# Optimization experiments

Hardware: AMD Instinct MI355X
Metric: run time of the kernel (lower is better)

The kernel has to match this reference:

```python
import jax, jax.numpy as jnp
import numpy as np

B, T, N = 512, 200, 256
ENC_G, ENC_C = 256, 256
C_DIM, G_DIM, U_DIM, F_DIM = 128, 256, 64, 64
CLIP = 5.0


def _gru(x, h, Wih, Whh, bih, bhh):
    # PyTorch nn.GRUCell math
    gi = x @ Wih.T + bih
    gh = h @ Whh.T + bhh
    ir, iz, inn = jnp.split(gi, 3, axis=-1)
    hr, hz, hn = jnp.split(gh, 3, axis=-1)
    r = jax.nn.sigmoid(ir + hr)
    z = jax.nn.sigmoid(iz + hz)
    n = jnp.tanh(inn + r * hn)
    return (1.0 - z) * n + z * h


def setup_inputs() -> dict:
    key = jax.random.key(0)
    ks = iter(jax.random.split(key, 64))

    def gru_p(i, h):
        return (jax.random.normal(next(ks), (3 * h, i)) * i ** -0.5,
                jax.random.normal(next(ks), (3 * h, h)) * h ** -0.5,
                jnp.zeros(3 * h), jnp.zeros(3 * h))

    def lin_p(i, o):
        return (jax.random.normal(next(ks), (o, i)) * i ** -0.5, jnp.zeros(o))

    inp = {}
    inp['x'] = jax.random.uniform(next(ks), (B, T, N))
    inp['eps_g0'] = jax.random.normal(next(ks), (B, G_DIM))
    inp['eps_u'] = jax.random.normal(next(ks), (B, T, U_DIM))
    for name, (i, h) in [('gf', (N, ENC_G)), ('gb', (N, ENC_G)),
                         ('cf', (N, ENC_C)), ('cb', (N, ENC_C)),
                         ('ct', (2 * ENC_C + F_DIM, C_DIM)), ('gn', (U_DIM, G_DIM))]:
        Wih, Whh, bih, bhh = gru_p(i, h)
        inp['Wih_' + name] = Wih; inp['Whh_' + name] = Whh
        inp['bih_' + name] = bih; inp['bhh_' + name] = bhh
    for name, (i, o) in [('g0m', (2 * ENC_G, G_DIM)), ('g0v', (2 * ENC_G, G_DIM)),
                         ('um', (C_DIM, U_DIM)), ('uv', (C_DIM, U_DIM)),
                         ('f', (G_DIM, F_DIM)), ('r', (F_DIM, N))]:
        W, b = lin_p(i, o)
        inp['W_' + name] = W; inp['b_' + name] = b
    return inp


def reference(x, eps_g0, eps_u,
              Wih_gf, Whh_gf, bih_gf, bhh_gf,
              Wih_gb, Whh_gb, bih_gb, bhh_gb,
              Wih_cf, Whh_cf, bih_cf, bhh_cf,
              Wih_cb, Whh_cb, bih_cb, bhh_cb,
              Wih_ct, Whh_ct, bih_ct, bhh_ct,
              Wih_gn, Whh_gn, bih_gn, bhh_gn,
              W_g0m, b_g0m, W_g0v, b_g0v,
              W_um, b_um, W_uv, b_uv,
              W_f, b_f, W_r, b_r):
    Bsz = x.shape[0]
    xs = x.transpose(1, 0, 2)  # [T, B, N]
    zg = jnp.zeros((Bsz, ENC_G), x.dtype)
    zc = jnp.zeros((Bsz, ENC_C), x.dtype)

    def make_enc(pg, pc):
        def step(carry, xt):
            hg, hc = carry
            hg = jnp.minimum(_gru(xt, hg, *pg), CLIP)   # clamp(max=clip_val)
            hc = jnp.minimum(_gru(xt, hc, *pc), CLIP)
            return (hg, hc), hc
        return step

    (hgf, _), hcf = jax.lax.scan(
        make_enc((Wih_gf, Whh_gf, bih_gf, bhh_gf), (Wih_cf, Whh_cf, bih_cf, bhh_cf)),
        (zg, zc), xs)
    (hgb, _), hcb = jax.lax.scan(
        make_enc((Wih_gb, Whh_gb, bih_gb, bhh_gb), (Wih_cb, Whh_cb, bih_cb, bhh_cb)),
        (zg, zc), xs[::-1])
    h_enc_g = jnp.concatenate([hgf, hgb], axis=-1)        # [B, 2*ENC_G]
    h_enc_c = jnp.concatenate([hcf, hcb[::-1]], axis=-1)  # [T, B, 2*ENC_C]

    g0_mean = h_enc_g @ W_g0m.T + b_g0m
    g0_logv = jnp.log(jnp.exp(h_enc_g @ W_g0v.T + b_g0v) + 1e-4)
    g0 = eps_g0 * jnp.exp(0.5 * g0_logv) + g0_mean

    f0 = g0 @ W_f.T + b_f
    hc0 = jnp.zeros((Bsz, C_DIM), x.dtype)

    def gen_step(carry, inp):
        h_c, g, f = carry
        henc_t, eps_t = inp
        cin = jnp.concatenate([henc_t, f], axis=-1)
        h_c = jnp.clip(_gru(cin, h_c, Wih_ct, Whh_ct, bih_ct, bhh_ct), 0.0, CLIP)
        um = h_c @ W_um.T + b_um
        ul = h_c @ W_uv.T + b_uv
        u = eps_t * jnp.exp(0.5 * ul) + um
        g = jnp.clip(_gru(u, g, Wih_gn, Whh_gn, bih_gn, bhh_gn), 0.0, CLIP)
        f = g @ W_f.T + b_f
        return (h_c, g, f), (um, ul, f)

    _, (u_means, u_logvs, factors) = jax.lax.scan(
        gen_step, (hc0, g0, f0), (h_enc_c, eps_u.transpose(1, 0, 2)))
    factors = factors.transpose(1, 0, 2)  # [B, T, F_DIM]
    rates = jnp.exp(jnp.clip(factors @ W_r.T + b_r, -CLIP, CLIP))
    return (g0_mean, g0_logv,
            u_means.transpose(1, 0, 2), u_logvs.transpose(1, 0, 2),
            factors, rates)
```

## Files before the change

### kernel.cpp

```cpp
#include <hip/hip_runtime.h>
#include <hip/hip_bf16.h>
#include <stdint.h>

typedef __bf16 bf16x8 __attribute__((ext_vector_type(8)));
typedef __bf16 bf16x4 __attribute__((ext_vector_type(4)));
typedef float  f32x4  __attribute__((ext_vector_type(4)));
typedef unsigned short u16x8 __attribute__((ext_vector_type(8)));

#define MFMA_B16(A_,B_,C_) __builtin_amdgcn_mfma_f32_16x16x32_bf16((A_),(B_),(C_),0,0,0)

static constexpr int TT = 200;
static constexpr int TC = 25;
static constexpr int NCH = 8;

static __device__ __forceinline__ float sig_f(float x){ return 1.f/(1.f+__expf(-x)); }
static __device__ __forceinline__ float tanh_f(float x){
  float e = __expf(-2.f*fabsf(x));
  float t = (1.f-e)/(1.f+e);
  return x<0.f ? -t : t;
}
static __device__ __forceinline__ float bf2f(unsigned short u){
  union{unsigned int i; float f;} v; v.i = ((unsigned)u)<<16; return v.f;
}
static __device__ __forceinline__ void pin8(bf16x8 &v){ asm volatile("" : "+v"(v)); }

static __device__ __forceinline__ int swz_off(int row, int col_bytes, int strideB){
  return (row*strideB + col_bytes) ^ ((row&7)<<4);
}
static __device__ __forceinline__ bf16x8 lds_rdA(const __bf16* buf, int row, int kt, int lq, int strideB){
  return *(const bf16x8*)((const char*)buf + swz_off(row, kt*64 + lq*16, strideB));
}
static __device__ __forceinline__ void lds_wr(__bf16* buf, int row, int dim, int strideB, float v){
  *(__bf16*)((char*)buf + swz_off(row, dim*2, strideB)) = (__bf16)v;
}
static __device__ __forceinline__ void lds_barrier(){
  asm volatile("s_waitcnt lgkmcnt(0)" ::: "memory");
  __builtin_amdgcn_s_barrier();
}

__global__ void cvt_bf16(const float* __restrict__ s, __bf16* __restrict__ d, int n){
  int i = blockIdx.x*blockDim.x + threadIdx.x;
  int st = gridDim.x*blockDim.x;
  for(; i<n; i+=st) d[i] = (__bf16)s[i];
}

__global__ void epsT_k(const float4* __restrict__ e, float4* __restrict__ o){
  const int total = 512*200*16;
  int j = blockIdx.x*blockDim.x + threadIdx.x;
  int st = gridDim.x*blockDim.x;
  for(; j<total; j+=st){
    int b = j/3200, rem = j - b*3200;
    int t = rem>>4, dq = rem&15;
    o[((size_t)t*512 + b)*16 + dq] = e[j];
  }
}

__global__ __launch_bounds__(256) void gi_gemm(const float* __restrict__ x,
                                               const __bf16* __restrict__ Wall,
                                               __bf16* __restrict__ gi, int t0){
  const int tid=threadIdx.x, w=tid>>6, l=tid&63, lr=l&15, lq=l>>4;
  const int cell = blockIdx.y;
  const bool fwd = (cell&1)==0;
  const int m0 = blockIdx.x*64;
  const int tloc = m0>>9, b0 = m0&511;
  const int tabs = fwd ? (t0+tloc) : (TT-1-(t0+tloc));
  const int brow = b0 + w*16 + lr;

  const float* xp = x + (size_t)brow*TT*256 + (size_t)tabs*256 + lq*8;
  bf16x8 a[8];
  #pragma unroll
  for(int kt=0;kt<8;kt++){
    float4 f0 = *(const float4*)(xp + kt*32);
    float4 f1 = *(const float4*)(xp + kt*32 + 4);
    bf16x8 v;
    v[0]=(__bf16)f0.x; v[1]=(__bf16)f0.y; v[2]=(__bf16)f0.z; v[3]=(__bf16)f0.w;
    v[4]=(__bf16)f1.x; v[5]=(__bf16)f1.y; v[6]=(__bf16)f1.z; v[7]=(__bf16)f1.w;
    a[kt]=v;
  }
  const __bf16* Wc = Wall + (size_t)cell*768*256;
  #pragma unroll 1
  for(int nt=0;nt<48;nt++){
    f32x4 acc={};
    const __bf16* bp = Wc + (size_t)(nt*16+lr)*256 + lq*8;
    #pragma unroll
    for(int kt=0;kt<8;kt++)
      acc = MFMA_B16(a[kt], *(const bf16x8*)(bp + kt*32), acc);
    bf16x4 pk;
    pk[0]=(__bf16)acc[0]; pk[1]=(__bf16)acc[1]; pk[2]=(__bf16)acc[2]; pk[3]=(__bf16)acc[3];
    *(bf16x4*)(gi + (((size_t)cell*TC + tloc)*768 + nt*16+lr)*512 + b0 + w*16 + lq*4) = pk;
  }
}

struct EncP{
  const __bf16* whh;
  const float*  bih[4];
  const float*  bhh[4];
  const __bf16* gi;
  __bf16* henc;
  float*  hcar;
  int t0;
};
__attribute__((amdgpu_waves_per_eu(2,2)))
__global__ __launch_bounds__(512) void enc_scan(EncP P){
  const int tid=threadIdx.x, w=tid>>6, l=tid&63, lr=l&15, lq=l>>4;
  const int cell=blockIdx.y, b0=blockIdx.x*16;
  const bool fwd = (cell&1)==0;
  const bool isC = cell>=2;
  const int dim0 = w*32;

  __shared__ __align__(16) __bf16 hA[2][16*256];
  __shared__ __align__(16) __bf16 giL[2][768*16];
  __shared__ float blds[1024];

  for(int d=tid; d<256; d+=512){
    blds[d]     = P.bih[cell][d]     + P.bhh[cell][d];
    blds[256+d] = P.bih[cell][256+d] + P.bhh[cell][256+d];
    blds[512+d] = P.bih[cell][512+d];
    blds[768+d] = P.bhh[cell][512+d];
  }
  const __bf16* Wh = P.whh + (size_t)cell*768*256;
  bf16x8 wreg[2][2][8];
  #pragma unroll
  for(int jt=0;jt<2;jt++)
    #pragma unroll
    for(int g=0;g<2;g++)
      #pragma unroll
      for(int kt=0;kt<8;kt++){
        wreg[jt][g][kt] = *(const bf16x8*)(Wh + (size_t)(g*256 + dim0 + jt*16 + lr)*256 + kt*32 + lq*8);
        pin8(wreg[jt][g][kt]);
      }
  f32x4 hold[2];
  #pragma unroll
  for(int jt=0;jt<2;jt++)
    #pragma unroll
    for(int rr=0;rr<4;rr++){
      float v = P.hcar[((size_t)cell*512 + b0 + lq*4+rr)*256 + dim0 + jt*16 + lr];
      hold[jt][rr] = v;
      lds_wr(hA[0], lq*4+rr, dim0+jt*16+lr, 512, v);
    }
  const int prow = w*96 + (l>>1), phal = l&1;
  const __bf16* gbase = P.gi + ((size_t)cell*TC*768 + prow)*512 + b0 + phal*8;
  u16x8 pf0, pf1, pf2;
  pf0 = *(const u16x8*)(gbase + (size_t)0*768*512 +  0*512);
  pf1 = *(const u16x8*)(gbase + (size_t)0*768*512 + 32*512);
  pf2 = *(const u16x8*)(gbase + (size_t)0*768*512 + 64*512);
  __syncthreads();
  {
    __bf16* gl = giL[0] + prow*16 + phal*8;
    *(u16x8*)(gl)        = pf0;
    *(u16x8*)(gl+32*16)  = pf1;
    *(u16x8*)(gl+64*16)  = pf2;
  }
  { int sn = 1 < TC ? 1 : TC-1;
    pf0 = *(const u16x8*)(gbase + (size_t)sn*768*512 +  0*512);
    pf1 = *(const u16x8*)(gbase + (size_t)sn*768*512 + 32*512);
    pf2 = *(const u16x8*)(gbase + (size_t)sn*768*512 + 64*512);
  }
  lds_barrier();

  int p=0, q=0;
  #pragma unroll 1
  for(int s=0;s<TC;s++){
    const int tglob = P.t0 + s;
    const int tx = fwd ? tglob : (TT-1-tglob);
    if(s+1<TC){
      __bf16* gl = giL[1-q] + prow*16 + phal*8;
      *(u16x8*)(gl)        = pf0;
      *(u16x8*)(gl+32*16)  = pf1;
      *(u16x8*)(gl+64*16)  = pf2;
    }
    { int sn = (s+2<TC) ? s+2 : TC-1;
      pf0 = *(const u16x8*)(gbase + (size_t)sn*768*512 +  0*512);
      pf1 = *(const u16x8*)(gbase + (size_t)sn*768*512 + 32*512);
      pf2 = *(const u16x8*)(gbase + (size_t)sn*768*512 + 64*512);
    }
    const __bf16* gq = giL[q];
    #pragma unroll
    for(int jt=0;jt<2;jt++){
      const int d = dim0 + jt*16 + lr;
      const __bf16* whN = Wh + (size_t)(512 + d)*256 + lq*8;
      f32x4 aR={}, aZ={}, aH={};
      #pragma unroll
      for(int kt=0;kt<8;kt++){
        bf16x8 frag = lds_rdA(hA[p], lr, kt, lq, 512);
        aR = MFMA_B16(frag, wreg[jt][0][kt], aR);
        aZ = MFMA_B16(frag, wreg[jt][1][kt], aZ);
        aH = MFMA_B16(frag, *(const bf16x8*)(whN + kt*32), aH);
      }
      ushort4 gR = *(const ushort4*)(gq + (0*256+d)*16 + lq*4);
      ushort4 gZ = *(const ushort4*)(gq + (1*256+d)*16 + lq*4);
      ushort4 gN = *(const ushort4*)(gq + (2*256+d)*16 + lq*4);
      const float bR=blds[d], bZ=blds[256+d], bI=blds[512+d], bH=blds[768+d];
      const unsigned short* uR=(const unsigned short*)&gR;
      const unsigned short* uZ=(const unsigned short*)&gZ;
      const unsigned short* uN=(const unsigned short*)&gN;
      #pragma unroll
      for(int rr=0;rr<4;rr++){
        float r = sig_f(aR[rr] + bf2f(uR[rr]) + bR);
        float z = sig_f(aZ[rr] + bf2f(uZ[rr]) + bZ);
        float nn= tanh_f(bf2f(uN[rr]) + bI + r*(aH[rr] + bH));
        float h = (1.f-z)*nn + z*hold[jt][rr];
        h = fminf(h, 5.f);
        hold[jt][rr] = h;
        lds_wr(hA[1-p], lq*4+rr, d, 512, h);
      }
    }
    if(isC){
      const int row = l>>2, dgrp = (l&3)*8;
      bf16x8 hv = *(const bf16x8*)((const char*)hA[1-p] +
                    ((row*512 + (dim0+dgrp)*2) ^ ((row&7)<<4)));
      *(bf16x8*)(P.henc + ((size_t)tx*512 + b0 + row)*512 + (cell==3?256:0) + dim0 + dgrp) = hv;
    }
    lds_barrier();
    p ^= 1; q ^= 1;
  }
  #pragma unroll
  for(int jt=0;jt<2;jt++)
    #pragma unroll
    for(int rr=0;rr<4;rr++)
      P.hcar[((size_t)cell*512 + b0 + lq*4+rr)*256 + dim0 + jt*16 + lr] = hold[jt][rr];
}

__global__ void g0_kernel(const float* __restrict__ hgf, const float* __restrict__ hgb,
                          const float* __restrict__ Wm, const float* __restrict__ bm,
                          const float* __restrict__ Wv, const float* __restrict__ bv,
                          const float* __restrict__ eps,
                          float* __restrict__ o_mean, float* __restrict__ o_logv,
                          float* __restrict__ g0){
  int j = blockIdx.x*blockDim.x + threadIdx.x;
  int b = j>>8, d = j&255;
  const float4* hf=(const float4*)(hgf + (size_t)b*256);
  const float4* hb=(const float4*)(hgb + (size_t)b*256);
  const float4* mp=(const float4*)(Wm + (size_t)d*512);
  const float4* vp=(const float4*)(Wv + (size_t)d*512);
  float am=0.f, av=0.f;
  #pragma unroll 4
  for(int k=0;k<64;k++){
    float4 h=hf[k], m=mp[k], v=vp[k];
    am += h.x*m.x + h.y*m.y + h.z*m.z + h.w*m.w;
    av += h.x*v.x + h.y*v.y + h.z*v.z + h.w*v.w;
  }
  #pragma unroll 4
  for(int k=0;k<64;k++){
    float4 h=hb[k], m=mp[64+k], v=vp[64+k];
    am += h.x*m.x + h.y*m.y + h.z*m.z + h.w*m.w;
    av += h.x*v.x + h.y*v.y + h.z*v.z + h.w*v.w;
  }
  float mean = am + bm[d];
  float ev   = __expf(av + bv[d]) + 1e-4f;
  float lv   = __logf(ev);
  o_mean[j]=mean; o_logv[j]=lv;
  g0[j] = eps[j]*sqrtf(ev) + mean;
}

__global__ __launch_bounds__(256,2) void gict_gemm(const __bf16* __restrict__ henc,
                                                   const __bf16* __restrict__ wct,
                                                   __bf16* __restrict__ gictT){
  const int tid=threadIdx.x, w=tid>>6, l=tid&63, lr=l&15, lq=l>>4;
  const int m0 = blockIdx.x*8 + w*2;
  bf16x8 a[2][16];
  #pragma unroll
  for(int m=0;m<2;m++){
    const __bf16* ap = henc + (size_t)((m0+m)*16 + lr)*512 + lq*8;
    #pragma unroll
    for(int kt=0;kt<16;kt++) a[m][kt] = *(const bf16x8*)(ap + kt*32);
  }
  #pragma unroll 1
  for(int nt=0;nt<24;nt++){
    f32x4 c0={}, c1={};
    const __bf16* bp = wct + (size_t)(nt*16+lr)*576 + lq*8;
    #pragma unroll
    for(int kt=0;kt<16;kt++){
      bf16x8 bb = *(const bf16x8*)(bp + kt*32);
      c0 = MFMA_B16(a[0][kt], bb, c0);
      c1 = MFMA_B16(a[1][kt], bb, c1);
    }
    #pragma unroll
    for(int m=0;m<2;m++){
      f32x4 c = m? c1 : c0;
      int R0 = (m0+m)*16 + lq*4;
      int t  = R0>>9, b = R0&511;
      bf16x4 pk;
      pk[0]=(__bf16)c[0]; pk[1]=(__bf16)c[1]; pk[2]=(__bf16)c[2]; pk[3]=(__bf16)c[3];
      *(bf16x4*)(gictT + ((size_t)t*384 + nt*16+lr)*512 + b) = pk;
    }
  }
}

struct GenP{
  const __bf16 *wct, *whh_ct, *wih_gn, *whh_gn, *w_um, *w_uv, *w_f;
  const float  *bih_ct, *bhh_ct, *bih_gn, *bhh_gn, *b_um, *b_uv, *b_f;
  const __bf16* gihT;
  const float*  g0;
  const float*  epsT;
  float *o_um, *o_ul, *o_f;
};
__attribute__((amdgpu_waves_per_eu(2,2)))
__global__ __launch_bounds__(512) void gen_scan(GenP P){
  const int tid=threadIdx.x, w=tid>>6, l=tid&63, lr=l&15, lq=l>>4;
  const int b0 = blockIdx.x*16;

  __shared__ __align__(16) __bf16 wgnL[768*64];
  __shared__ __align__(16) __bf16 hcA[2][16*128];
  __shared__ __align__(16) __bf16 gA [2][16*256];
  __shared__ __align__(16) __bf16 uA [16*64];
  __shared__ __align__(16) __bf16 fA [16*64];

  for(int c=tid; c<6144; c+=512){
    int row = c>>3, part = c&7;
    bf16x8 v = *(const bf16x8*)(P.wih_gn + (size_t)row*64 + part*8);
    *(bf16x8*)((char*)wgnL + ((row*128 + part*16) ^ ((row&7)<<4))) = v;
  }
  bf16x8 wrz[2][2][8];
  #pragma unroll
  for(int jt=0;jt<2;jt++)
    #pragma unroll
    for(int g=0;g<2;g++)
      #pragma unroll
      for(int kt=0;kt<8;kt++){
        wrz[jt][g][kt] = *(const bf16x8*)(P.whh_gn + (size_t)(g*256 + w*32 + jt*16 + lr)*256 + kt*32 + lq*8);
        pin8(wrz[jt][g][kt]);
      }

  const int dct = w*16 + lr;
  const int duu = (w&3)*16 + lr;
  const float bctR = P.bih_ct[dct]     + P.bhh_ct[dct];
  const float bctZ = P.bih_ct[128+dct] + P.bhh_ct[128+dct];
  const float bctI = P.bih_ct[256+dct];
  const float bctH = P.bhh_ct[256+dct];
  float bgnR[2], bgnZ[2], bgnI[2], bgnH[2];
  #pragma unroll
  for(int jt=0;jt<2;jt++){
    int d = w*32 + jt*16 + lr;
    bgnR[jt] = P.bih_gn[d]     + P.bhh_gn[d];
    bgnZ[jt] = P.bih_gn[256+d] + P.bhh_gn[256+d];
    bgnI[jt] = P.bih_gn[512+d];
    bgnH[jt] = P.bhh_gn[512+d];
  }
  const float bum = P.b_um[duu], buv = P.b_uv[duu], bff = P.b_f[duu];

  f32x4 gC[2], hcC;
  hcC = (f32x4){};
  #pragma unroll
  for(int jt=0;jt<2;jt++)
    #pragma unroll
    for(int rr=0;rr<4;rr++){
      float v = P.g0[(size_t)(b0+lq*4+rr)*256 + w*32 + jt*16 + lr];
      gC[jt][rr] = v;
      lds_wr(gA[0], lq*4+rr, w*32+jt*16+lr, 512, v);
    }
  for(int i=tid;i<16*128;i+=512) hcA[0][i] = (__bf16)0.f;
  __syncthreads();
  if(w>=4){
    f32x4 fa={};
    #pragma unroll
    for(int kt=0;kt<8;kt++){
      bf16x8 gf = lds_rdA(gA[0], lr, kt, lq, 512);
      fa = MFMA_B16(gf, *(const bf16x8*)(P.w_f + (size_t)duu*256 + kt*32 + lq*8), fa);
    }
    #pragma unroll
    for(int rr=0;rr<4;rr++) lds_wr(fA, lq*4+rr, duu, 128, fa[rr]+bff);
  }
  ushort4 gpR, gpZ, gpN; float epf[4];
  gpR = *(const ushort4*)(P.gihT + ((size_t)0*384 +       dct)*512 + b0 + lq*4);
  gpZ = *(const ushort4*)(P.gihT + ((size_t)0*384 + 128 + dct)*512 + b0 + lq*4);
  gpN = *(const ushort4*)(P.gihT + ((size_t)0*384 + 256 + dct)*512 + b0 + lq*4);
  if(w<4){
    #pragma unroll
    for(int rr=0;rr<4;rr++) epf[rr] = P.epsT[((size_t)0*512 + b0+lq*4+rr)*64 + duu];
  }
  bf16x8 cwh[3][4];
  #pragma unroll
  for(int g=0;g<3;g++)
    #pragma unroll
    for(int kt=0;kt<4;kt++)
      cwh[g][kt] = *(const bf16x8*)(P.whh_ct + (size_t)(g*128+dct)*128 + kt*32 + lq*8);
  __syncthreads();

  int pc=0, pg=0;
  #pragma unroll 1
  for(int t=0;t<TT;t++){
    {
      bf16x8 ff0 = lds_rdA(fA, lr, 0, lq, 128);
      bf16x8 ff1 = lds_rdA(fA, lr, 1, lq, 128);
      bf16x8 hp0 = lds_rdA(hcA[pc], lr, 0, lq, 256);
      bf16x8 hp1 = lds_rdA(hcA[pc], lr, 1, lq, 256);
      bf16x8 hp2 = lds_rdA(hcA[pc], lr, 2, lq, 256);
      bf16x8 hp3 = lds_rdA(hcA[pc], lr, 3, lq, 256);
      f32x4 aR={}, aZ={}, aI={}, aH={};
      #pragma unroll
      for(int g=0;g<3;g++){
        const __bf16* wif = P.wct + (size_t)(g*128+dct)*576 + 512 + lq*8;
        bf16x8 wf0 = *(const bf16x8*)(wif);
        bf16x8 wf1 = *(const bf16x8*)(wif + 32);
        if(g==0){
          aR = MFMA_B16(ff0,wf0,aR); aR = MFMA_B16(ff1,wf1,aR);
          aR = MFMA_B16(hp0,cwh[0][0],aR); aR = MFMA_B16(hp1,cwh[0][1],aR);
          aR = MFMA_B16(hp2,cwh[0][2],aR); aR = MFMA_B16(hp3,cwh[0][3],aR);
        }else if(g==1){
          aZ = MFMA_B16(ff0,wf0,aZ); aZ = MFMA_B16(ff1,wf1,aZ);
          aZ = MFMA_B16(hp0,cwh[1][0],aZ); aZ = MFMA_B16(hp1,cwh[1][1],aZ);
          aZ = MFMA_B16(hp2,cwh[1][2],aZ); aZ = MFMA_B16(hp3,cwh[1][3],aZ);
        }else{
          aI = MFMA_B16(ff0,wf0,aI); aI = MFMA_B16(ff1,wf1,aI);
          aH = MFMA_B16(hp0,cwh[2][0],aH); aH = MFMA_B16(hp1,cwh[2][1],aH);
          aH = MFMA_B16(hp2,cwh[2][2],aH); aH = MFMA_B16(hp3,cwh[2][3],aH);
        }
      }
      const unsigned short* uR=(const unsigned short*)&gpR;
      const unsigned short* uZ=(const unsigned short*)&gpZ;
      const unsigned short* uN=(const unsigned short*)&gpN;
      #pragma unroll
      for(int rr=0;rr<4;rr++){
        float r = sig_f(aR[rr] + bf2f(uR[rr]) + bctR);
        float z = sig_f(aZ[rr] + bf2f(uZ[rr]) + bctZ);
        float nn= tanh_f(aI[rr] + bf2f(uN[rr]) + bctI + r*(aH[rr] + bctH));
        float h = (1.f-z)*nn + z*hcC[rr];
        h = fminf(fmaxf(h,0.f), 5.f);
        hcC[rr] = h;
        lds_wr(hcA[1-pc], lq*4+rr, dct, 256, h);
      }
    }
    lds_barrier();

    if(w<4){
      bf16x8 hn0 = lds_rdA(hcA[1-pc], lr, 0, lq, 256);
      bf16x8 hn1 = lds_rdA(hcA[1-pc], lr, 1, lq, 256);
      bf16x8 hn2 = lds_rdA(hcA[1-pc], lr, 2, lq, 256);
      bf16x8 hn3 = lds_rdA(hcA[1-pc], lr, 3, lq, 256);
      f32x4 am={}, av={};
      const __bf16* wm = P.w_um + (size_t)duu*128 + lq*8;
      const __bf16* wv = P.w_uv + (size_t)duu*128 + lq*8;
      am = MFMA_B16(hn0, *(const bf16x8*)(wm   ), am);
      am = MFMA_B16(hn1, *(const bf16x8*)(wm+32), am);
      am = MFMA_B16(hn2, *(const bf16x8*)(wm+64), am);
      am = MFMA_B16(hn3, *(const bf16x8*)(wm+96), am);
      av = MFMA_B16(hn0, *(const bf16x8*)(wv   ), av);
      av = MFMA_B16(hn1, *(const bf16x8*)(wv+32), av);
      av = MFMA_B16(hn2, *(const bf16x8*)(wv+64), av);
      av = MFMA_B16(hn3, *(const bf16x8*)(wv+96), av);
      #pragma unroll
      for(int rr=0;rr<4;rr++){
        const int row = lq*4+rr;
        float um = am[rr] + bum;
        float ul = av[rr] + buv;
        size_t oi = ((size_t)(b0+row)*TT + t)*64 + duu;
        P.o_um[oi] = um;
        P.o_ul[oi] = ul;
        float u = epf[rr]*__expf(0.5f*ul) + um;
        lds_wr(uA, row, duu, 128, u);
      }
    }
    bf16x8 wn0[8];
    #pragma unroll
    for(int kt=0;kt<8;kt++)
      wn0[kt] = *(const bf16x8*)(P.whh_gn + (size_t)(512 + w*32 + lr)*256 + kt*32 + lq*8);
    lds_barrier();

    {
      const int tn = (t+1<TT)? t+1 : TT-1;
      gpR = *(const ushort4*)(P.gihT + ((size_t)tn*384 +       dct)*512 + b0 + lq*4);
      gpZ = *(const ushort4*)(P.gihT + ((size_t)tn*384 + 128 + dct)*512 + b0 + lq*4);
      gpN = *(const ushort4*)(P.gihT + ((size_t)tn*384 + 256 + dct)*512 + b0 + lq*4);
      if(w<4){
        #pragma unroll
        for(int rr=0;rr<4;rr++) epf[rr] = P.epsT[((size_t)tn*512 + b0+lq*4+rr)*64 + duu];
      }
      bf16x8 uf0 = lds_rdA(uA, lr, 0, lq, 128);
      bf16x8 uf1 = lds_rdA(uA, lr, 1, lq, 128);
      #pragma unroll
      for(int jt=0;jt<2;jt++){
        const int dg = w*32 + jt*16 + lr;
        bf16x8 wn[8];
        if(jt==0){
          #pragma unroll
          for(int kt=0;kt<8;kt++) wn[kt] = wn0[kt];
        }else{
          #pragma unroll
          for(int kt=0;kt<8;kt++)
            wn[kt] = *(const bf16x8*)(P.whh_gn + (size_t)(512 + dg)*256 + kt*32 + lq*8);
        }
        f32x4 aR={}, aZ={}, aI={}, aH={};
        #pragma unroll
        for(int g=0;g<3;g++){
          const int row = g*256 + dg;
          bf16x8 w0 = *(const bf16x8*)((const char*)wgnL + ((row*128 +  0 + lq*16) ^ ((row&7)<<4)));
          bf16x8 w1 = *(const bf16x8*)((const char*)wgnL + ((row*128 + 64 + lq*16) ^ ((row&7)<<4)));
          if(g==0){ aR = MFMA_B16(uf0,w0,aR); aR = MFMA_B16(uf1,w1,aR); }
          else if(g==1){ aZ = MFMA_B16(uf0,w0,aZ); aZ = MFMA_B16(uf1,w1,aZ); }
          else { aI = MFMA_B16(uf0,w0,aI); aI = MFMA_B16(uf1,w1,aI); }
        }
        #pragma unroll
        for(int kt=0;kt<8;kt++){
          bf16x8 gf = lds_rdA(gA[pg], lr, kt, lq, 512);
          aR = MFMA_B16(gf, wrz[jt][0][kt], aR);
          aZ = MFMA_B16(gf, wrz[jt][1][kt], aZ);
          aH = MFMA_B16(gf, wn[kt], aH);
        }
        #pragma unroll
        for(int rr=0;rr<4;rr++){
          float r = sig_f(aR[rr] + bgnR[jt]);
          float z = sig_f(aZ[rr] + bgnZ[jt]);
          float nn= tanh_f(aI[rr] + bgnI[jt] + r*(aH[rr] + bgnH[jt]));
          float gv = (1.f-z)*nn + z*gC[jt][rr];
          gv = fminf(fmaxf(gv,0.f), 5.f);
          gC[jt][rr] = gv;
          lds_wr(gA[1-pg], lq*4+rr, dg, 512, gv);
        }
      }
    }
    lds_barrier();

    if(w>=4){
      f32x4 fa={};
      const __bf16* wfp = P.w_f + (size_t)duu*256 + lq*8;
      #pragma unroll
      for(int kt=0;kt<8;kt++){
        bf16x8 gf = lds_rdA(gA[1-pg], lr, kt, lq, 512);
        fa = MFMA_B16(gf, *(const bf16x8*)(wfp + kt*32), fa);
      }
      #pragma unroll
      for(int rr=0;rr<4;rr++){
        const int row = lq*4+rr;
        float v = fa[rr] + bff;
        P.o_f[((size_t)(b0+row)*TT + t)*64 + duu] = v;
        lds_wr(fA, row, duu, 128, v);
      }
    }
    #pragma unroll
    for(int g=0;g<3;g++)
      #pragma unroll
      for(int kt=0;kt<4;kt++)
        cwh[g][kt] = *(const bf16x8*)(P.whh_ct + (size_t)(g*128+dct)*128 + kt*32 + lq*8);
    lds_barrier();
    pc ^= 1; pg ^= 1;
  }
}

__global__ void rates_k(const float* __restrict__ fac, const float* __restrict__ Wr,
                        const float* __restrict__ br, float* __restrict__ out){
  const int total = 512*200*256;
  int i = blockIdx.x*blockDim.x + threadIdx.x;
  int st = gridDim.x*blockDim.x;
  for(; i<total; i+=st){
    int row = i>>8, n = i&255;
    const float4* fp=(const float4*)(fac + (size_t)row*64);
    const float4* wp=(const float4*)(Wr  + (size_t)n*64);
    float a = 0.f;
    #pragma unroll
    for(int k=0;k<16;k++){
      float4 f=fp[k], ww=wp[k];
      a += f.x*ww.x + f.y*ww.y + f.z*ww.z + f.w*ww.w;
    }
    a += br[n];
    a = fminf(fmaxf(a, -5.f), 5.f);
    out[i] = __expf(a);
  }
}

extern "C" void kernel_launch(void* const* d_in, const int* in_sizes, int n_in,
                              void* d_out, int out_size, void* d_ws, size_t ws_size,
                              hipStream_t stream){
  (void)in_sizes; (void)n_in; (void)out_size; (void)ws_size;
  const float* x      = (const float*)d_in[0];
  const float* eps_g0 = (const float*)d_in[1];
  const float* eps_u  = (const float*)d_in[2];
  const float* Wih_f[6]; const float* Whh_f[6]; const float* bih[6]; const float* bhh[6];
  for(int c=0;c<6;c++){
    Wih_f[c]=(const float*)d_in[3+4*c]; Whh_f[c]=(const float*)d_in[4+4*c];
    bih[c]  =(const float*)d_in[5+4*c]; bhh[c]  =(const float*)d_in[6+4*c];
  }
  const float* W_g0m=(const float*)d_in[27]; const float* b_g0m=(const float*)d_in[28];
  const float* W_g0v=(const float*)d_in[29]; const float* b_g0v=(const float*)d_in[30];
  const float* W_um =(const float*)d_in[31]; const float* b_um =(const float*)d_in[32];
  const float* W_uv =(const float*)d_in[33]; const float* b_uv =(const float*)d_in[34];
  const float* W_f  =(const float*)d_in[35]; const float* b_f  =(const float*)d_in[36];
  const float* W_r  =(const float*)d_in[37]; const float* b_r  =(const float*)d_in[38];

  char* ws = (char*)d_ws; size_t off = 0;
  auto alloc = [&](size_t bytes)->char*{
    char* p = ws + off; off = (off + bytes + 255) & ~(size_t)255; return p;
  };
  __bf16* wencall = (__bf16*)alloc((size_t)4*768*256*2);
  __bf16* whhall  = (__bf16*)alloc((size_t)4*768*256*2);
  __bf16* wct_b   = (__bf16*)alloc((size_t)384*576*2);
  __bf16* whhct_b = (__bf16*)alloc((size_t)384*128*2);
  __bf16* wihgn_b = (__bf16*)alloc((size_t)768*64*2);
  __bf16* whhgn_b = (__bf16*)alloc((size_t)768*256*2);
  __bf16* wum_b   = (__bf16*)alloc((size_t)64*128*2);
  __bf16* wuv_b   = (__bf16*)alloc((size_t)64*128*2);
  __bf16* wf_b    = (__bf16*)alloc((size_t)64*256*2);
  __bf16* henc    = (__bf16*)alloc((size_t)200*512*512*2);
  __bf16* gi_buf  = (__bf16*)alloc((size_t)4*TC*768*512*2);
  float*  hcar    = (float*)alloc((size_t)4*512*256*4);
  float*  g0buf   = (float*)alloc((size_t)512*256*4);

  for(int c=0;c<4;c++){
    cvt_bf16<<<128,256,0,stream>>>(Wih_f[c], wencall + (size_t)c*768*256, 768*256);
    cvt_bf16<<<128,256,0,stream>>>(Whh_f[c], whhall  + (size_t)c*768*256, 768*256);
  }
  cvt_bf16<<<128,256,0,stream>>>(Wih_f[4], wct_b,   384*576);
  cvt_bf16<<<64 ,256,0,stream>>>(Whh_f[4], whhct_b, 384*128);
  cvt_bf16<<<64 ,256,0,stream>>>(Wih_f[5], wihgn_b, 768*64);
  cvt_bf16<<<128,256,0,stream>>>(Whh_f[5], whhgn_b, 768*256);
  cvt_bf16<<<32 ,256,0,stream>>>(W_um, wum_b, 64*128);
  cvt_bf16<<<32 ,256,0,stream>>>(W_uv, wuv_b, 64*128);
  cvt_bf16<<<32 ,256,0,stream>>>(W_f,  wf_b,  64*256);
  hipMemsetAsync(hcar, 0, (size_t)4*512*256*4, stream);

  EncP ep;
  ep.whh = whhall;
  for(int c=0;c<4;c++){ ep.bih[c]=bih[c]; ep.bhh[c]=bhh[c]; }
  ep.gi = gi_buf; ep.henc = henc; ep.hcar = hcar;
  for(int k=0;k<NCH;k++){
    gi_gemm<<<dim3((512*TC)/64,4),256,0,stream>>>(x, wencall, gi_buf, k*TC);
    ep.t0 = k*TC;
    enc_scan<<<dim3(32,4),512,0,stream>>>(ep);
  }

  float* out = (float*)d_out;
  float* o_mean = out;
  float* o_logv = out + 131072;
  float* o_um   = out + 262144;
  float* o_ul   = out + 6815744;
  float* o_f    = out + 13369344;
  float* o_r    = out + 19922944;

  g0_kernel<<<512,256,0,stream>>>(hcar + 0, hcar + (size_t)1*512*256,
                                  W_g0m,b_g0m, W_g0v,b_g0v, eps_g0,
                                  o_mean,o_logv, g0buf);
  gict_gemm<<<800,256,0,stream>>>(henc, wct_b, gi_buf);

  float* epsT = (float*)henc;
  epsT_k<<<2048,256,0,stream>>>((const float4*)eps_u, (float4*)epsT);

  GenP gp;
  gp.wct=wct_b; gp.whh_ct=whhct_b; gp.wih_gn=wihgn_b; gp.whh_gn=whhgn_b;
  gp.w_um=wum_b; gp.w_uv=wuv_b; gp.w_f=wf_b;
  gp.bih_ct=bih[4]; gp.bhh_ct=bhh[4]; gp.bih_gn=bih[5]; gp.bhh_gn=bhh[5];
  gp.b_um=b_um; gp.b_uv=b_uv; gp.b_f=b_f;
  gp.gihT=gi_buf; gp.g0=g0buf; gp.epsT=epsT;
  gp.o_um=o_um; gp.o_ul=o_ul; gp.o_f=o_f;
  gen_scan<<<32,512,0,stream>>>(gp);

  rates_k<<<8192,256,0,stream>>>(o_f, W_r, b_r, o_r);
}
```

Before: 7.337 ms.

## Stream recurrent weights from global instead of pinning in registers; move biases to LDS

Removes the register-resident recurrent weight fragments (and the waves_per_eu(2,2) pin) in both the encoder and generator scan kernels. Weights are now reloaded from global/L2 every timestep in grouped batches, and biases are staged in shared memory rather than held in registers. The intent is to cut VGPR pressure and allow the compiler more freedom or higher occupancy. The cost is much more global/L2 weight traffic on the latency-critical recurrent step.

Result: slower. 8.938 ms (+21.8%).

```diff
diff --git a/kernel.cpp b/kernel.cpp
--- a/kernel.cpp
+++ b/kernel.cpp
@@ -22,8 +22,6 @@
 static __device__ __forceinline__ float bf2f(unsigned short u){
   union{unsigned int i; float f;} v; v.i = ((unsigned)u)<<16; return v.f;
 }
-static __device__ __forceinline__ void pin8(bf16x8 &v){ asm volatile("" : "+v"(v)); }
-
 static __device__ __forceinline__ int swz_off(int row, int col_bytes, int strideB){
   return (row*strideB + col_bytes) ^ ((row&7)<<4);
 }
@@ -100,7 +98,6 @@
   float*  hcar;
   int t0;
 };
-__attribute__((amdgpu_waves_per_eu(2,2)))
 __global__ __launch_bounds__(512) void enc_scan(EncP P){
   const int tid=threadIdx.x, w=tid>>6, l=tid&63, lr=l&15, lq=l>>4;
   const int cell=blockIdx.y, b0=blockIdx.x*16;
@@ -119,16 +116,6 @@
     blds[768+d] = P.bhh[cell][512+d];
   }
   const __bf16* Wh = P.whh + (size_t)cell*768*256;
-  bf16x8 wreg[2][2][8];
-  #pragma unroll
-  for(int jt=0;jt<2;jt++)
-    #pragma unroll
-    for(int g=0;g<2;g++)
-      #pragma unroll
-      for(int kt=0;kt<8;kt++){
-        wreg[jt][g][kt] = *(const bf16x8*)(Wh + (size_t)(g*256 + dim0 + jt*16 + lr)*256 + kt*32 + lq*8);
-        pin8(wreg[jt][g][kt]);
-      }
   f32x4 hold[2];
   #pragma unroll
   for(int jt=0;jt<2;jt++)
@@ -175,17 +162,36 @@
       pf2 = *(const u16x8*)(gbase + (size_t)sn*768*512 + 64*512);
     }
     const __bf16* gq = giL[q];
+    bf16x8 hf[8];
+    #pragma unroll
+    for(int kt=0;kt<8;kt++) hf[kt] = lds_rdA(hA[p], lr, kt, lq, 512);
     #pragma unroll
     for(int jt=0;jt<2;jt++){
       const int d = dim0 + jt*16 + lr;
-      const __bf16* whN = Wh + (size_t)(512 + d)*256 + lq*8;
       f32x4 aR={}, aZ={}, aH={};
-      #pragma unroll
-      for(int kt=0;kt<8;kt++){
-        bf16x8 frag = lds_rdA(hA[p], lr, kt, lq, 512);
-        aR = MFMA_B16(frag, wreg[jt][0][kt], aR);
-        aZ = MFMA_B16(frag, wreg[jt][1][kt], aZ);
-        aH = MFMA_B16(frag, *(const bf16x8*)(whN + kt*32), aH);
+      {
+        const __bf16* wp = Wh + (size_t)d*256 + lq*8;
+        bf16x8 wg[8];
+        #pragma unroll
+        for(int kt=0;kt<8;kt++) wg[kt] = *(const bf16x8*)(wp + kt*32);
+        #pragma unroll
+        for(int kt=0;kt<8;kt++) aR = MFMA_B16(hf[kt], wg[kt], aR);
+      }
+      {
+        const __bf16* wp = Wh + (size_t)(256+d)*256 + lq*8;
+        bf16x8 wg[8];
+        #pragma unroll
+        for(int kt=0;kt<8;kt++) wg[kt] = *(const bf16x8*)(wp + kt*32);
+        #pragma unroll
+        for(int kt=0;kt<8;kt++) aZ = MFMA_B16(hf[kt], wg[kt], aZ);
+      }
+      {
+        const __bf16* wp = Wh + (size_t)(512+d)*256 + lq*8;
+        bf16x8 wg[8];
+        #pragma unroll
+        for(int kt=0;kt<8;kt++) wg[kt] = *(const bf16x8*)(wp + kt*32);
+        #pragma unroll
+        for(int kt=0;kt<8;kt++) aH = MFMA_B16(hf[kt], wg[kt], aH);
       }
       ushort4 gR = *(const ushort4*)(gq + (0*256+d)*16 + lq*4);
       ushort4 gZ = *(const ushort4*)(gq + (1*256+d)*16 + lq*4);
@@ -295,7 +301,6 @@
   const float*  epsT;
   float *o_um, *o_ul, *o_f;
 };
-__attribute__((amdgpu_waves_per_eu(2,2)))
 __global__ __launch_bounds__(512) void gen_scan(GenP P){
   const int tid=threadIdx.x, w=tid>>6, l=tid&63, lr=l&15, lq=l>>4;
   const int b0 = blockIdx.x*16;
@@ -305,39 +310,33 @@
   __shared__ __align__(16) __bf16 gA [2][16*256];
   __shared__ __align__(16) __bf16 uA [16*64];
   __shared__ __align__(16) __bf16 fA [16*64];
+  __shared__ float bldsG[1728];
 
   for(int c=tid; c<6144; c+=512){
     int row = c>>3, part = c&7;
     bf16x8 v = *(const bf16x8*)(P.wih_gn + (size_t)row*64 + part*8);
     *(bf16x8*)((char*)wgnL + ((row*128 + part*16) ^ ((row&7)<<4))) = v;
   }
-  bf16x8 wrz[2][2][8];
-  #pragma unroll
-  for(int jt=0;jt<2;jt++)
-    #pragma unroll
-    for(int g=0;g<2;g++)
-      #pragma unroll
-      for(int kt=0;kt<8;kt++){
-        wrz[jt][g][kt] = *(const bf16x8*)(P.whh_gn + (size_t)(g*256 + w*32 + jt*16 + lr)*256 + kt*32 + lq*8);
-        pin8(wrz[jt][g][kt]);
-      }
+  for(int d=tid; d<128; d+=512){
+    bldsG[d]     = P.bih_ct[d]     + P.bhh_ct[d];
+    bldsG[128+d] = P.bih_ct[128+d] + P.bhh_ct[128+d];
+    bldsG[256+d] = P.bih_ct[256+d];
+    bldsG[384+d] = P.bhh_ct[256+d];
+  }
+  for(int d=tid; d<256; d+=512){
+    bldsG[512+d]  = P.bih_gn[d]     + P.bhh_gn[d];
+    bldsG[768+d]  = P.bih_gn[256+d] + P.bhh_gn[256+d];
+    bldsG[1024+d] = P.bih_gn[512+d];
+    bldsG[1280+d] = P.bhh_gn[512+d];
+  }
+  for(int d=tid; d<64; d+=512){
+    bldsG[1536+d] = P.b_um[d];
+    bldsG[1600+d] = P.b_uv[d];
+    bldsG[1664+d] = P.b_f[d];
+  }
 
   const int dct = w*16 + lr;
   const int duu = (w&3)*16 + lr;
-  const float bctR = P.bih_ct[dct]     + P.bhh_ct[dct];
-  const float bctZ = P.bih_ct[128+dct] + P.bhh_ct[128+dct];
-  const float bctI = P.bih_ct[256+dct];
-  const float bctH = P.bhh_ct[256+dct];
-  float bgnR[2], bgnZ[2], bgnI[2], bgnH[2];
-  #pragma unroll
-  for(int jt=0;jt<2;jt++){
-    int d = w*32 + jt*16 + lr;
-    bgnR[jt] = P.bih_gn[d]     + P.bhh_gn[d];
-    bgnZ[jt] = P.bih_gn[256+d] + P.bhh_gn[256+d];
-    bgnI[jt] = P.bih_gn[512+d];
-    bgnH[jt] = P.bhh_gn[512+d];
-  }
-  const float bum = P.b_um[duu], buv = P.b_uv[duu], bff = P.b_f[duu];
 
   f32x4 gC[2], hcC;
   hcC = (f32x4){};
@@ -353,11 +352,13 @@
   __syncthreads();
   if(w>=4){
     f32x4 fa={};
+    const __bf16* wfp = P.w_f + (size_t)duu*256 + lq*8;
     #pragma unroll
     for(int kt=0;kt<8;kt++){
       bf16x8 gf = lds_rdA(gA[0], lr, kt, lq, 512);
-      fa = MFMA_B16(gf, *(const bf16x8*)(P.w_f + (size_t)duu*256 + kt*32 + lq*8), fa);
-    }
+      fa = MFMA_B16(gf, *(const bf16x8*)(wfp + kt*32), fa);
+    }
+    float bff = bldsG[1664+duu];
     #pragma unroll
     for(int rr=0;rr<4;rr++) lds_wr(fA, lq*4+rr, duu, 128, fa[rr]+bff);
   }
@@ -369,12 +370,6 @@
     #pragma unroll
     for(int rr=0;rr<4;rr++) epf[rr] = P.epsT[((size_t)0*512 + b0+lq*4+rr)*64 + duu];
   }
-  bf16x8 cwh[3][4];
-  #pragma unroll
-  for(int g=0;g<3;g++)
-    #pragma unroll
-    for(int kt=0;kt<4;kt++)
-      cwh[g][kt] = *(const bf16x8*)(P.whh_ct + (size_t)(g*128+dct)*128 + kt*32 + lq*8);
   __syncthreads();
 
   int pc=0, pg=0;
@@ -388,33 +383,45 @@
       bf16x8 hp2 = lds_rdA(hcA[pc], lr, 2, lq, 256);
       bf16x8 hp3 = lds_rdA(hcA[pc], lr, 3, lq, 256);
       f32x4 aR={}, aZ={}, aI={}, aH={};
-      #pragma unroll
-      for(int g=0;g<3;g++){
-        const __bf16* wif = P.wct + (size_t)(g*128+dct)*576 + 512 + lq*8;
-        bf16x8 wf0 = *(const bf16x8*)(wif);
-        bf16x8 wf1 = *(const bf16x8*)(wif + 32);
-        if(g==0){
-          aR = MFMA_B16(ff0,wf0,aR); aR = MFMA_B16(ff1,wf1,aR);
-          aR = MFMA_B16(hp0,cwh[0][0],aR); aR = MFMA_B16(hp1,cwh[0][1],aR);
-          aR = MFMA_B16(hp2,cwh[0][2],aR); aR = MFMA_B16(hp3,cwh[0][3],aR);
-        }else if(g==1){
-          aZ = MFMA_B16(ff0,wf0,aZ); aZ = MFMA_B16(ff1,wf1,aZ);
-          aZ = MFMA_B16(hp0,cwh[1][0],aZ); aZ = MFMA_B16(hp1,cwh[1][1],aZ);
-          aZ = MFMA_B16(hp2,cwh[1][2],aZ); aZ = MFMA_B16(hp3,cwh[1][3],aZ);
-        }else{
-          aI = MFMA_B16(ff0,wf0,aI); aI = MFMA_B16(ff1,wf1,aI);
-          aH = MFMA_B16(hp0,cwh[2][0],aH); aH = MFMA_B16(hp1,cwh[2][1],aH);
-          aH = MFMA_B16(hp2,cwh[2][2],aH); aH = MFMA_B16(hp3,cwh[2][3],aH);
-        }
-      }
+      {
+        const __bf16* wif = P.wct    + (size_t)dct*576 + 512 + lq*8;
+        const __bf16* whc = P.whh_ct + (size_t)dct*128 + lq*8;
+        bf16x8 a0=*(const bf16x8*)wif, a1=*(const bf16x8*)(wif+32);
+        bf16x8 h0=*(const bf16x8*)whc, h1=*(const bf16x8*)(whc+32);
+        bf16x8 h2=*(const bf16x8*)(whc+64), h3=*(const bf16x8*)(whc+96);
+        aR=MFMA_B16(ff0,a0,aR); aR=MFMA_B16(ff1,a1,aR);
+        aR=MFMA_B16(hp0,h0,aR); aR=MFMA_B16(hp1,h1,aR);
+        aR=MFMA_B16(hp2,h2,aR); aR=MFMA_B16(hp3,h3,aR);
+      }
+      {
+        const __bf16* wif = P.wct    + (size_t)(128+dct)*576 + 512 + lq*8;
+        const __bf16* whc = P.whh_ct + (size_t)(128+dct)*128 + lq*8;
+        bf16x8 a0=*(const bf16x8*)wif, a1=*(const bf16x8*)(wif+32);
+        bf16x8 h0=*(const bf16x8*)whc, h1=*(const bf16x8*)(whc+32);
+        bf16x8 h2=*(const bf16x8*)(whc+64), h3=*(const bf16x8*)(whc+96);
+        aZ=MFMA_B16(ff0,a0,aZ); aZ=MFMA_B16(ff1,a1,aZ);
+        aZ=MFMA_B16(hp0,h0,aZ); aZ=MFMA_B16(hp1,h1,aZ);
+        aZ=MFMA_B16(hp2,h2,aZ); aZ=MFMA_B16(hp3,h3,aZ);
+      }
+      {
+        const __bf16* wif = P.wct    + (size_t)(256+dct)*576 + 512 + lq*8;
+        const __bf16* whc = P.whh_ct + (size_t)(256+dct)*128 + lq*8;
+        bf16x8 a0=*(const bf16x8*)wif, a1=*(const bf16x8*)(wif+32);
+        bf16x8 h0=*(const bf16x8*)whc, h1=*(const bf16x8*)(whc+32);
+        bf16x8 h2=*(const bf16x8*)(whc+64), h3=*(const bf16x8*)(whc+96);
+        aI=MFMA_B16(ff0,a0,aI); aI=MFMA_B16(ff1,a1,aI);
+        aH=MFMA_B16(hp0,h0,aH); aH=MFMA_B16(hp1,h1,aH);
+        aH=MFMA_B16(hp2,h2,aH); aH=MFMA_B16(hp3,h3,aH);
+      }
+      const float bR=bldsG[dct], bZ=bldsG[128+dct], bI=bldsG[256+dct], bH=bldsG[384+dct];
       const unsigned short* uR=(const unsigned short*)&gpR;
       const unsigned short* uZ=(const unsigned short*)&gpZ;
       const unsigned short* uN=(const unsigned short*)&gpN;
       #pragma unroll
       for(int rr=0;rr<4;rr++){
-        float r = sig_f(aR[rr] + bf2f(uR[rr]) + bctR);
-        float z = sig_f(aZ[rr] + bf2f(uZ[rr]) + bctZ);
-        float nn= tanh_f(aI[rr] + bf2f(uN[rr]) + bctI + r*(aH[rr] + bctH));
+        float r = sig_f(aR[rr] + bf2f(uR[rr]) + bR);
+        float z = sig_f(aZ[rr] + bf2f(uZ[rr]) + bZ);
+        float nn= tanh_f(aI[rr] + bf2f(uN[rr]) + bI + r*(aH[rr] + bH));
         float h = (1.f-z)*nn + z*hcC[rr];
         h = fminf(fmaxf(h,0.f), 5.f);
         hcC[rr] = h;
@@ -429,16 +436,21 @@
       bf16x8 hn2 = lds_rdA(hcA[1-pc], lr, 2, lq, 256);
       bf16x8 hn3 = lds_rdA(hcA[1-pc], lr, 3, lq, 256);
       f32x4 am={}, av={};
-      const __bf16* wm = P.w_um + (size_t)duu*128 + lq*8;
-      const __bf16* wv = P.w_uv + (size_t)duu*128 + lq*8;
-      am = MFMA_B16(hn0, *(const bf16x8*)(wm   ), am);
-      am = MFMA_B16(hn1, *(const bf16x8*)(wm+32), am);
-      am = MFMA_B16(hn2, *(const bf16x8*)(wm+64), am);
-      am = MFMA_B16(hn3, *(const bf16x8*)(wm+96), am);
-      av = MFMA_B16(hn0, *(const bf16x8*)(wv   ), av);
-      av = MFMA_B16(hn1, *(const bf16x8*)(wv+32), av);
-      av = MFMA_B16(hn2, *(const bf16x8*)(wv+64), av);
-      av = MFMA_B16(hn3, *(const bf16x8*)(wv+96), av);
+      {
+        const __bf16* wm = P.w_um + (size_t)duu*128 + lq*8;
+        bf16x8 m0=*(const bf16x8*)wm, m1=*(const bf16x8*)(wm+32);
+        bf16x8 m2=*(const bf16x8*)(wm+64), m3=*(const bf16x8*)(wm+96);
+        am=MFMA_B16(hn0,m0,am); am=MFMA_B16(hn1,m1,am);
+        am=MFMA_B16(hn2,m2,am); am=MFMA_B16(hn3,m3,am);
+      }
+      {
+        const __bf16* wv = P.w_uv + (size_t)duu*128 + lq*8;
+        bf16x8 v0=*(const bf16x8*)wv, v1=*(const bf16x8*)(wv+32);
+        bf16x8 v2=*(const bf16x8*)(wv+64), v3=*(const bf16x8*)(wv+96);
+        av=MFMA_B16(hn0,v0,av); av=MFMA_B16(hn1,v1,av);
+        av=MFMA_B16(hn2,v2,av); av=MFMA_B16(hn3,v3,av);
+      }
+      const float bum = bldsG[1536+duu], buv = bldsG[1600+duu];
       #pragma unroll
       for(int rr=0;rr<4;rr++){
         const int row = lq*4+rr;
@@ -451,10 +463,6 @@
         lds_wr(uA, row, duu, 128, u);
       }
     }
-    bf16x8 wn0[8];
-    #pragma unroll
-    for(int kt=0;kt<8;kt++)
-      wn0[kt] = *(const bf16x8*)(P.whh_gn + (size_t)(512 + w*32 + lr)*256 + kt*32 + lq*8);
     lds_barrier();
 
     {
@@ -466,42 +474,56 @@
         #pragma unroll
         for(int rr=0;rr<4;rr++) epf[rr] = P.epsT[((size_t)tn*512 + b0+lq*4+rr)*64 + duu];
       }
-      bf16x8 uf0 = lds_rdA(uA, lr, 0, lq, 128);
-      bf16x8 uf1 = lds_rdA(uA, lr, 1, lq, 128);
       #pragma unroll
       for(int jt=0;jt<2;jt++){
         const int dg = w*32 + jt*16 + lr;
-        bf16x8 wn[8];
-        if(jt==0){
+        f32x4 aR={}, aZ={}, aI={}, aH={};
+        {
+          bf16x8 uf0 = lds_rdA(uA, lr, 0, lq, 128);
+          bf16x8 uf1 = lds_rdA(uA, lr, 1, lq, 128);
           #pragma unroll
-          for(int kt=0;kt<8;kt++) wn[kt] = wn0[kt];
-        }else{
+          for(int g=0;g<3;g++){
+            const int row = g*256 + dg;
+            bf16x8 w0 = *(const bf16x8*)((const char*)wgnL + ((row*128 +  0 + lq*16) ^ ((row&7)<<4)));
+            bf16x8 w1 = *(const bf16x8*)((const char*)wgnL + ((row*128 + 64 + lq*16) ^ ((row&7)<<4)));
+            if(g==0){ aR = MFMA_B16(uf0,w0,aR); aR = MFMA_B16(uf1,w1,aR); }
+            else if(g==1){ aZ = MFMA_B16(uf0,w0,aZ); aZ = MFMA_B16(uf1,w1,aZ); }
+            else { aI = MFMA_B16(uf0,w0,aI); aI = MFMA_B16(uf1,w1,aI); }
+          }
+        }
+        bf16x8 gfr[8];
+        #pragma unroll
+        for(int kt=0;kt<8;kt++) gfr[kt] = lds_rdA(gA[pg], lr, kt, lq, 512);
+        {
+          const __bf16* wp = P.whh_gn + (size_t)dg*256 + lq*8;
+          bf16x8 wg[8];
           #pragma unroll
-          for(int kt=0;kt<8;kt++)
-            wn[kt] = *(const bf16x8*)(P.whh_gn + (size_t)(512 + dg)*256 + kt*32 + lq*8);
+          for(int kt=0;kt<8;kt++) wg[kt] = *(const bf16x8*)(wp + kt*32);
+          #pragma unroll
+          for(int kt=0;kt<8;kt++) aR = MFMA_B16(gfr[kt], wg[kt], aR);
         }
-        f32x4 aR={}, aZ={}, aI={}, aH={};
-        #pragma unroll
-        for(int g=0;g<3;g++){
-          const int row = g*256 + dg;
-          bf16x8 w0 = *(const bf16x8*)((const char*)wgnL + ((row*128 +  0 + lq*16) ^ ((row&7)<<4)));
-          bf16x8 w1 = *(const bf16x8*)((const char*)wgnL + ((row*128 + 64 + lq*16) ^ ((row&7)<<4)));
-          if(g==0){ aR = MFMA_B16(uf0,w0,aR); aR = MFMA_B16(uf1,w1,aR); }
-          else if(g==1){ aZ = MFMA_B16(uf0,w0,aZ); aZ = MFMA_B16(uf1,w1,aZ); }
-          else { aI = MFMA_B16(uf0,w0,aI); aI = MFMA_B16(uf1,w1,aI); }
+        {
+          const __bf16* wp = P.whh_gn + (size_t)(256+dg)*256 + lq*8;
+          bf16x8 wg[8];
+          #pragma unroll
+          for(int kt=0;kt<8;kt++) wg[kt] = *(const bf16x8*)(wp + kt*32);
+          #pragma unroll
+          for(int kt=0;kt<8;kt++) aZ = MFMA_B16(gfr[kt], wg[kt], aZ);
         }
-        #pragma unroll
-        for(int kt=0;kt<8;kt++){
-          bf16x8 gf = lds_rdA(gA[pg], lr, kt, lq, 512);
-          aR = MFMA_B16(gf, wrz[jt][0][kt], aR);
-          aZ = MFMA_B16(gf, wrz[jt][1][kt], aZ);
-          aH = MFMA_B16(gf, wn[kt], aH);
+        {
+          const __bf16* wp = P.whh_gn + (size_t)(512+dg)*256 + lq*8;
+          bf16x8 wg[8];
+          #pragma unroll
+          for(int kt=0;kt<8;kt++) wg[kt] = *(const bf16x8*)(wp + kt*32);
+          #pragma unroll
+          for(int kt=0;kt<8;kt++) aH = MFMA_B16(gfr[kt], wg[kt], aH);
         }
+        const float bR=bldsG[512+dg], bZ=bldsG[768+dg], bI=bldsG[1024+dg], bH=bldsG[1280+dg];
         #pragma unroll
         for(int rr=0;rr<4;rr++){
-          float r = sig_f(aR[rr] + bgnR[jt]);
-          float z = sig_f(aZ[rr] + bgnZ[jt]);
-          float nn= tanh_f(aI[rr] + bgnI[jt] + r*(aH[rr] + bgnH[jt]));
+          float r = sig_f(aR[rr] + bR);
+          float z = sig_f(aZ[rr] + bZ);
+          float nn= tanh_f(aI[rr] + bI + r*(aH[rr] + bH));
           float gv = (1.f-z)*nn + z*gC[jt][rr];
           gv = fminf(fmaxf(gv,0.f), 5.f);
           gC[jt][rr] = gv;
@@ -514,11 +536,15 @@
     if(w>=4){
       f32x4 fa={};
       const __bf16* wfp = P.w_f + (size_t)duu*256 + lq*8;
+      bf16x8 wfg[8];
+      #pragma unroll
+      for(int kt=0;kt<8;kt++) wfg[kt] = *(const bf16x8*)(wfp + kt*32);
       #pragma unroll
       for(int kt=0;kt<8;kt++){
         bf16x8 gf = lds_rdA(gA[1-pg], lr, kt, lq, 512);
-        fa = MFMA_B16(gf, *(const bf16x8*)(wfp + kt*32), fa);
-      }
+        fa = MFMA_B16(gf, wfg[kt], fa);
+      }
+      const float bff = bldsG[1664+duu];
       #pragma unroll
       for(int rr=0;rr<4;rr++){
         const int row = lq*4+rr;
@@ -527,11 +553,6 @@
         lds_wr(fA, row, duu, 128, v);
       }
     }
-    #pragma unroll
-    for(int g=0;g<3;g++)
-      #pragma unroll
-      for(int kt=0;kt<4;kt++)
-        cwh[g][kt] = *(const bf16x8*)(P.whh_ct + (size_t)(g*128+dct)*128 + kt*32 + lq*8);
     lds_barrier();
     pc ^= 1; pg ^= 1;
   }
```
